# Optimization experiments

Hardware: AMD Instinct MI355X
Metric: run time of the kernel (lower is better)

## Reference

```python
import jax, jax.numpy as jnp
import numpy as np

N_NODES = 50000
N_EDGES = 1_600_000
DIMS = [3, 4096, 1024, 256, 64, 16]  # conv1..conv5 in/out widths


def setup_inputs() -> dict:
    key = jax.random.key(0)
    ks = jax.random.split(key, 2 + 2 * 6)
    x = jax.random.normal(ks[0], (N_NODES, DIMS[0]), jnp.float32)
    edge_index = jax.random.randint(ks[1], (2, N_EDGES), 0, N_NODES, jnp.int64)
    inp = {"x": x, "edge_index": edge_index}
    # GCNConv weights (lin has no bias fused; bias added after aggregation)
    for i in range(5):
        fi, fo = DIMS[i], DIMS[i + 1]
        inp[f"W{i+1}"] = jax.random.normal(ks[2 + 2 * i], (fi, fo), jnp.float32) / np.float32(np.sqrt(fi))
        inp[f"b{i+1}"] = jnp.zeros((fo,), jnp.float32)
    # final Linear(num_classes, 3)
    inp["Wl"] = jax.random.normal(ks[12], (DIMS[5], 3), jnp.float32) / np.float32(np.sqrt(DIMS[5]))
    inp["bl"] = jnp.zeros((3,), jnp.float32)
    return inp


def _gcn_layer(x, W, b, src, dst, dinv):
    """GCNConv: h = XW; out = D^-1/2 (A+I) D^-1/2 h + b (self-loops included)."""
    h = x @ W  # [N, out]
    norm = dinv[src] * dinv[dst]  # [E]
    agg = jax.ops.segment_sum(h[src] * norm[:, None], dst, num_segments=N_NODES)
    # self-loop term: norm_ii = dinv[i]^2
    return agg + h * (dinv * dinv)[:, None] + b


def reference(x, edge_index, W1, b1, W2, b2, W3, b3, W4, b4, W5, b5, Wl, bl):
    src, dst = edge_index[0], edge_index[1]
    # degree with self-loops (edge weights = 1), computed on target nodes
    deg = jax.ops.segment_sum(jnp.ones((N_EDGES,), x.dtype), dst, num_segments=N_NODES) + 1.0
    dinv = jax.lax.rsqrt(deg)
    h = _gcn_layer(x, W1, b1, src, dst, dinv)
    h = jax.nn.relu(h)  # dropout = identity in eval
    h = _gcn_layer(h, W2, b2, src, dst, dinv)
    h = jax.nn.relu(h)
    h = _gcn_layer(h, W3, b3, src, dst, dinv)
    h = jax.nn.relu(h)
    h = _gcn_layer(h, W4, b4, src, dst, dinv)
    h = jax.nn.relu(h)
    h = _gcn_layer(h, W5, b5, src, dst, dinv)
    # scatter_mean with broadcast index [0] -> global mean pool to [1, C]
    pooled = jnp.mean(h, axis=0, keepdims=True)
    return pooled @ Wl + bl  # [1, 3]
```

## Files before the change

### kernel.cpp

```cpp
#include <hip/hip_runtime.h>
#include <stdint.h>

#define NN 50000
#define NE 1600000

typedef _Float16 f16;
typedef __attribute__((ext_vector_type(8))) _Float16 h8;
typedef __attribute__((ext_vector_type(4))) _Float16 h4v;
typedef __attribute__((ext_vector_type(4))) float f32x4;
typedef __attribute__((ext_vector_type(2))) float f32x2;

union PackU { unsigned int u; f16 h[2]; };
union Pack4 { uint2 v; f16 h[4]; };
union Pack8 { uint4 v; f16 h[8]; };

__device__ __forceinline__ void storev(float* p, float v) { *p = v; }
__device__ __forceinline__ void storev(f16* p, float v) { *p = (f16)v; }

__device__ __forceinline__ unsigned char f2fp8(float v) {
    int pk = __builtin_amdgcn_cvt_pk_fp8_f32(v, v, 0, false);
    return (unsigned char)(pk & 0xff);
}

__global__ __launch_bounds__(256) void zero_int_kernel(int* __restrict__ p, int n) {
    int i = blockIdx.x * 256 + threadIdx.x;
    if (i < n) p[i] = 0;
}

__global__ __launch_bounds__(256) void count_kernel(const int* __restrict__ dst,
                                                    int* __restrict__ deg, int nE) {
    int e = blockIdx.x * 256 + threadIdx.x;
    if (e < nE) atomicAdd(&deg[dst[e]], 1);
}

__global__ __launch_bounds__(256) void dinv_kernel(const int* __restrict__ deg,
                                                   float* __restrict__ dinv, int n) {
    int i = blockIdx.x * 256 + threadIdx.x;
    if (i < n) dinv[i] = rsqrtf((float)deg[i] + 1.0f);
}

__global__ __launch_bounds__(256) void scan1_kernel(const int* __restrict__ cnt,
                                                    int* __restrict__ rs,
                                                    int* __restrict__ bsum, int n) {
    __shared__ int sm[256];
    int b = blockIdx.x, t = threadIdx.x, i = b * 256 + t;
    int v = (i < n) ? cnt[i] : 0;
    sm[t] = v;
    __syncthreads();
    for (int off = 1; off < 256; off <<= 1) {
        int x = 0;
        if (t >= off) x = sm[t - off];
        __syncthreads();
        if (t >= off) sm[t] += x;
        __syncthreads();
    }
    if (i < n) rs[i] = sm[t] - v;
    if (t == 255) bsum[b] = sm[255];
}

__global__ __launch_bounds__(256) void scan2_kernel(int* __restrict__ bsum,
                                                    int* __restrict__ rs, int nb, int n) {
    __shared__ int sm[256];
    int t = threadIdx.x;
    int v = (t < nb) ? bsum[t] : 0;
    sm[t] = v;
    __syncthreads();
    for (int off = 1; off < 256; off <<= 1) {
        int x = 0;
        if (t >= off) x = sm[t - off];
        __syncthreads();
        if (t >= off) sm[t] += x;
        __syncthreads();
    }
    if (t < nb) bsum[t] = sm[t] - v;
    if (t == 255) rs[n] = sm[255];
}

__global__ __launch_bounds__(256) void scan3_kernel(int* __restrict__ rs,
                                                    const int* __restrict__ bsum, int n) {
    int i = blockIdx.x * 256 + threadIdx.x;
    if (i < n) rs[i] += bsum[blockIdx.x];
}

__global__ __launch_bounds__(256) void fill_kernel(const int* __restrict__ src,
                                                   const int* __restrict__ dst,
                                                   const int* __restrict__ rs,
                                                   int* __restrict__ cur,
                                                   int* __restrict__ csr, int nE) {
    int e = blockIdx.x * 256 + threadIdx.x;
    if (e < nE) {
        int d = dst[e];
        int p = rs[d] + atomicAdd(&cur[d], 1);
        csr[p] = src[e];
    }
}

__global__ __launch_bounds__(256) void pack_w1_kernel(const float* __restrict__ W1,
                                                      const float* __restrict__ b1,
                                                      float* __restrict__ w1p) {
    int k = blockIdx.x * 256 + threadIdx.x;
    if (k < 4096) {
        w1p[k * 4 + 0] = W1[k];
        w1p[k * 4 + 1] = W1[4096 + k];
        w1p[k * 4 + 2] = W1[8192 + k];
        w1p[k * 4 + 3] = b1[k];
    }
}

__global__ __launch_bounds__(256) void tconv_kernel(const float* __restrict__ W,
                                                    f16* __restrict__ Wt,
                                                    int K, int N) {
    __shared__ float tile[32][33];
    int kb = blockIdx.y * 32, nb = blockIdx.x * 32;
    int tx = threadIdx.x & 31, ty = threadIdx.x >> 5;
    for (int r = ty; r < 32; r += 8)
        tile[r][tx] = W[(size_t)(kb + r) * N + nb + tx];
    __syncthreads();
    for (int r = ty; r < 32; r += 8)
        Wt[(size_t)(nb + r) * K + kb + tx] = (f16)tile[tx][r];
}

template <int F, int TPN, bool RELU, bool BIAS, typename OutT>
__global__ __launch_bounds__(256) void agg_kernel(const float* __restrict__ t,
                                                  const float* __restrict__ dinv,
                                                  const int* __restrict__ rs,
                                                  const int* __restrict__ csr,
                                                  const float* __restrict__ bias,
                                                  OutT* __restrict__ out, int out_ld,
                                                  int nNodes) {
    constexpr int NPB = 256 / TPN;
    constexpr int C   = F / TPN;
    static_assert(TPN * C == F, "F must be TPN*C");
    int node = blockIdx.x * NPB + (int)threadIdx.x / TPN;
    if (node >= nNodes) return;
    int lane = (int)threadIdx.x % TPN;

    float acc[C];
#pragma unroll
    for (int c = 0; c < C; ++c) acc[c] = 0.f;

    int e0 = rs[node], e1 = rs[node + 1];
    for (int e = e0; e < e1; ++e) {
        int s = csr[e];
        float w = dinv[s];
        const float* tr = t + (size_t)s * F;
#pragma unroll
        for (int c = 0; c < C; ++c) acc[c] += w * tr[lane + c * TPN];
    }
    float di = dinv[node];
    const float* ti = t + (size_t)node * F;
    OutT* oi = out + (size_t)node * out_ld;
#pragma unroll
    for (int c = 0; c < C; ++c) {
        int col = lane + c * TPN;
        float v = di * acc[c] + di * di * ti[col];
        if (BIAS) v += bias[col];
        if (RELU) v = fmaxf(v, 0.f);
        storev(oi + col, v);
    }
}

template <bool RELU>
__global__ __launch_bounds__(256) void agg_fp8_1024(const unsigned char* __restrict__ t,
                                                    const float* __restrict__ dinv,
                                                    const int* __restrict__ rs,
                                                    const int* __restrict__ csr,
                                                    const float* __restrict__ bias,
                                                    f16* __restrict__ out, int nNodes) {
    int node = blockIdx.x * 4 + ((int)threadIdx.x >> 6);
    if (node >= nNodes) return;
    int lane = (int)threadIdx.x & 63;

    float acc[16];
#pragma unroll
    for (int j = 0; j < 16; ++j) acc[j] = 0.f;

    int e0 = rs[node], e1 = rs[node + 1];
    int e = e0;
    for (; e + 1 < e1; e += 2) {
        int s0 = csr[e], s1 = csr[e + 1];
        float w0 = dinv[s0], w1 = dinv[s1];
        uint4 u0 = ((const uint4*)(t + (size_t)s0 * 1024))[lane];
        uint4 u1 = ((const uint4*)(t + (size_t)s1 * 1024))[lane];
        const unsigned int uw0[4] = {u0.x, u0.y, u0.z, u0.w};
        const unsigned int uw1[4] = {u1.x, u1.y, u1.z, u1.w};
#pragma unroll
        for (int q = 0; q < 4; ++q) {
            f32x2 l0 = __builtin_amdgcn_cvt_pk_f32_fp8((int)uw0[q], false);
            f32x2 h0 = __builtin_amdgcn_cvt_pk_f32_fp8((int)uw0[q], true);
            f32x2 l1 = __builtin_amdgcn_cvt_pk_f32_fp8((int)uw1[q], false);
            f32x2 h1 = __builtin_amdgcn_cvt_pk_f32_fp8((int)uw1[q], true);
            acc[q * 4 + 0] += w0 * l0.x + w1 * l1.x;
            acc[q * 4 + 1] += w0 * l0.y + w1 * l1.y;
            acc[q * 4 + 2] += w0 * h0.x + w1 * h1.x;
            acc[q * 4 + 3] += w0 * h0.y + w1 * h1.y;
        }
    }
    if (e < e1) {
        int s0 = csr[e];
        float w0 = dinv[s0];
        uint4 u0 = ((const uint4*)(t + (size_t)s0 * 1024))[lane];
        const unsigned int uw0[4] = {u0.x, u0.y, u0.z, u0.w};
#pragma unroll
        for (int q = 0; q < 4; ++q) {
            f32x2 l0 = __builtin_amdgcn_cvt_pk_f32_fp8((int)uw0[q], false);
            f32x2 h0 = __builtin_amdgcn_cvt_pk_f32_fp8((int)uw0[q], true);
            acc[q * 4 + 0] += w0 * l0.x;
            acc[q * 4 + 1] += w0 * l0.y;
            acc[q * 4 + 2] += w0 * h0.x;
            acc[q * 4 + 3] += w0 * h0.y;
        }
    }
    float di = dinv[node], di2 = di * di;
    uint4 us = ((const uint4*)(t + (size_t)node * 1024))[lane];
    const unsigned int uws[4] = {us.x, us.y, us.z, us.w};
    Pack8 o0, o1;
#pragma unroll
    for (int q = 0; q < 4; ++q) {
        f32x2 sl = __builtin_amdgcn_cvt_pk_f32_fp8((int)uws[q], false);
        f32x2 sh = __builtin_amdgcn_cvt_pk_f32_fp8((int)uws[q], true);
        float4 b = *(const float4*)(bias + 16 * lane + q * 4);
        float v0 = di * acc[q * 4 + 0] + di2 * sl.x + b.x;
        float v1 = di * acc[q * 4 + 1] + di2 * sl.y + b.y;
        float v2 = di * acc[q * 4 + 2] + di2 * sh.x + b.z;
        float v3 = di * acc[q * 4 + 3] + di2 * sh.y + b.w;
        if (RELU) {
            v0 = fmaxf(v0, 0.f); v1 = fmaxf(v1, 0.f);
            v2 = fmaxf(v2, 0.f); v3 = fmaxf(v3, 0.f);
        }
        Pack8& dst8 = (q < 2) ? o0 : o1;
        int base = (q & 1) * 4;
        dst8.h[base + 0] = (f16)v0;
        dst8.h[base + 1] = (f16)v1;
        dst8.h[base + 2] = (f16)v2;
        dst8.h[base + 3] = (f16)v3;
    }
    uint4* orow = (uint4*)(out + (size_t)node * 1024 + 16 * lane);
    orow[0] = o0.v;
    orow[1] = o1.v;
}

template <bool RELU>
__global__ __launch_bounds__(256) void agg_fp8_256(const unsigned char* __restrict__ t,
                                                   int in_ld,
                                                   const float* __restrict__ dinv,
                                                   const int* __restrict__ rs,
                                                   const int* __restrict__ csr,
                                                   const float* __restrict__ bias,
                                                   f16* __restrict__ out,
                                                   int out_ld, int nNodes) {
    int node = blockIdx.x * 4 + ((int)threadIdx.x >> 6);
    if (node >= nNodes) return;
    int lane = (int)threadIdx.x & 63;

    float acc0 = 0.f, acc1 = 0.f, acc2 = 0.f, acc3 = 0.f;
    int e0 = rs[node], e1 = rs[node + 1];
    int e = e0;
    for (; e + 1 < e1; e += 2) {
        int s0 = csr[e], s1 = csr[e + 1];
        float w0 = dinv[s0], w1 = dinv[s1];
        unsigned int u0 = ((const unsigned int*)(t + (size_t)s0 * in_ld))[lane];
        unsigned int u1 = ((const unsigned int*)(t + (size_t)s1 * in_ld))[lane];
        f32x2 l0 = __builtin_amdgcn_cvt_pk_f32_fp8((int)u0, false);
        f32x2 h0 = __builtin_amdgcn_cvt_pk_f32_fp8((int)u0, true);
        f32x2 l1 = __builtin_amdgcn_cvt_pk_f32_fp8((int)u1, false);
        f32x2 h1 = __builtin_amdgcn_cvt_pk_f32_fp8((int)u1, true);
        acc0 += w0 * l0.x + w1 * l1.x;
        acc1 += w0 * l0.y + w1 * l1.y;
        acc2 += w0 * h0.x + w1 * h1.x;
        acc3 += w0 * h0.y + w1 * h1.y;
    }
    if (e < e1) {
        int s0 = csr[e];
        float w0 = dinv[s0];
        unsigned int u0 = ((const unsigned int*)(t + (size_t)s0 * in_ld))[lane];
        f32x2 l0 = __builtin_amdgcn_cvt_pk_f32_fp8((int)u0, false);
        f32x2 h0 = __builtin_amdgcn_cvt_pk_f32_fp8((int)u0, true);
        acc0 += w0 * l0.x;
        acc1 += w0 * l0.y;
        acc2 += w0 * h0.x;
        acc3 += w0 * h0.y;
    }
    float di = dinv[node], di2 = di * di;
    unsigned int us = ((const unsigned int*)(t + (size_t)node * in_ld))[lane];
    f32x2 sl = __builtin_amdgcn_cvt_pk_f32_fp8((int)us, false);
    f32x2 sh = __builtin_amdgcn_cvt_pk_f32_fp8((int)us, true);
    float4 b = *(const float4*)(bias + 4 * lane);
    float v0 = di * acc0 + di2 * sl.x + b.x;
    float v1 = di * acc1 + di2 * sl.y + b.y;
    float v2 = di * acc2 + di2 * sh.x + b.z;
    float v3 = di * acc3 + di2 * sh.y + b.w;
    if (RELU) {
        v0 = fmaxf(v0, 0.f); v1 = fmaxf(v1, 0.f);
        v2 = fmaxf(v2, 0.f); v3 = fmaxf(v3, 0.f);
    }
    Pack4 pk;
    pk.h[0] = (f16)v0; pk.h[1] = (f16)v1; pk.h[2] = (f16)v2; pk.h[3] = (f16)v3;
    *(uint2*)(out + (size_t)node * out_ld + 4 * lane) = pk.v;
}

#define LDSTR 40

__global__ __launch_bounds__(512, 4) void gemm12_mfma4(const float* __restrict__ aggx,
                                                       const float* __restrict__ w1p,
                                                       const f16* __restrict__ Bt,
                                                       unsigned char* __restrict__ t2) {
    __shared__ f16 As[128 * LDSTR] __attribute__((aligned(16)));
    __shared__ f16 Bs[256 * LDSTR] __attribute__((aligned(16)));
    int tid = threadIdx.x;
    int m0  = blockIdx.x * 128;
    int n0c = blockIdx.y * 256;

    int mg = tid >> 3;
    int kg = tid & 7;
    float a0[2], a1[2], a2[2];
#pragma unroll
    for (int j = 0; j < 2; ++j) {
        int gm = m0 + mg * 2 + j;
        if (gm < NN) {
            a0[j] = aggx[gm * 3 + 0];
            a1[j] = aggx[gm * 3 + 1];
            a2[j] = aggx[gm * 3 + 2];
        } else {
            a0[j] = a1[j] = a2[j] = 0.f;
        }
    }

    int brow = tid >> 1;
    int bkof = (tid & 1) * 16;
    const f16* bbase = Bt + (size_t)(n0c + brow) * 4096 + bkof;

    int lane   = tid & 63;
    int wv     = tid >> 6;
    int wm     = (wv >> 2) * 64;
    int wn     = (wv & 3) * 64;
    int fr_m   = lane & 15;
    int khalf8 = (lane >> 4) * 8;

    h8 pb0 = *(const h8*)(bbase);
    h8 pb1 = *(const h8*)(bbase + 8);

    f32x4 acc[4][4];
#pragma unroll
    for (int i = 0; i < 4; ++i)
#pragma unroll
        for (int j = 0; j < 4; ++j) acc[i][j] = (f32x4){0.f, 0.f, 0.f, 0.f};

    for (int k0 = 0; k0 < 4096; k0 += 32) {
        int kb = k0 + kg * 4;
        float4 wk0 = *(const float4*)(w1p + (size_t)(kb + 0) * 4);
        float4 wk1 = *(const float4*)(w1p + (size_t)(kb + 1) * 4);
        float4 wk2 = *(const float4*)(w1p + (size_t)(kb + 2) * 4);
        float4 wk3 = *(const float4*)(w1p + (size_t)(kb + 3) * 4);
#pragma unroll
        for (int j = 0; j < 2; ++j) {
            float h0 = fmaxf(a0[j] * wk0.x + a1[j] * wk0.y + a2[j] * wk0.z + wk0.w, 0.f);
            float h1 = fmaxf(a0[j] * wk1.x + a1[j] * wk1.y + a2[j] * wk1.z + wk1.w, 0.f);
            float h2 = fmaxf(a0[j] * wk2.x + a1[j] * wk2.y + a2[j] * wk2.z + wk2.w, 0.f);
            float h3 = fmaxf(a0[j] * wk3.x + a1[j] * wk3.y + a2[j] * wk3.z + wk3.w, 0.f);
            Pack4 pk;
            pk.h[0] = (f16)h0; pk.h[1] = (f16)h1; pk.h[2] = (f16)h2; pk.h[3] = (f16)h3;
            *(uint2*)(&As[(mg * 2 + j) * LDSTR + kg * 4]) = pk.v;
        }
        *(h8*)(&Bs[brow * LDSTR + bkof]) = pb0;
        *(h8*)(&Bs[brow * LDSTR + bkof + 8]) = pb1;
        __syncthreads();

        int kn = k0 + 32;
        if (kn < 4096) {
            pb0 = *(const h8*)(bbase + kn);
            pb1 = *(const h8*)(bbase + kn + 8);
        }

        h8 af[4];
#pragma unroll
        for (int mt = 0; mt < 4; ++mt)
            af[mt] = *(const h8*)(&As[(wm + mt * 16 + fr_m) * LDSTR + khalf8]);
#pragma unroll
        for (int nt = 0; nt < 4; ++nt) {
            h8 bf = *(const h8*)(&Bs[(wn + nt * 16 + fr_m) * LDSTR + khalf8]);
#pragma unroll
            for (int mt = 0; mt < 4; ++mt)
                acc[mt][nt] = __builtin_amdgcn_mfma_f32_16x16x32_f16(af[mt], bf, acc[mt][nt], 0, 0, 0);
        }
        __syncthreads();
    }

#pragma unroll
    for (int mt = 0; mt < 4; ++mt) {
#pragma unroll
        for (int reg = 0; reg < 4; ++reg) {
            int gm = m0 + wm + mt * 16 + (lane >> 4) * 4 + reg;
            if (gm < NN) {
                unsigned char* orow = t2 + (size_t)gm * 1024 + n0c + wn + fr_m;
#pragma unroll
                for (int nt = 0; nt < 4; ++nt)
                    orow[nt * 16] = f2fp8(acc[mt][nt][reg]);
            }
        }
    }
}

__global__ __launch_bounds__(256) void gemm_mfma(const f16* __restrict__ A, int lda,
                                                 const f16* __restrict__ Bt, int K,
                                                 unsigned char* __restrict__ C, int ldc,
                                                 int M) {
    __shared__ f16 As[128 * LDSTR] __attribute__((aligned(16)));
    __shared__ f16 Bs[128 * LDSTR] __attribute__((aligned(16)));
    int tid = threadIdx.x;
    int m0 = blockIdx.y * 128;
    int n0 = blockIdx.x * 128;

    int row = tid >> 1;
    int kof = (tid & 1) * 16;
    int am  = m0 + row;
    if (am > M - 1) am = M - 1;

    int lane   = tid & 63;
    int wv     = tid >> 6;
    int fr_m   = lane & 15;
    int khalf8 = (lane >> 4) * 8;

    const f16* abase = A + (size_t)am * lda + kof;
    const f16* bbase = Bt + (size_t)(n0 + row) * K + kof;

    h8 pa0 = *(const h8*)(abase);
    h8 pa1 = *(const h8*)(abase + 8);
    h8 pb0 = *(const h8*)(bbase);
    h8 pb1 = *(const h8*)(bbase + 8);

    f32x4 acc[2][8];
#pragma unroll
    for (int i = 0; i < 2; ++i)
#pragma unroll
        for (int j = 0; j < 8; ++j) acc[i][j] = (f32x4){0.f, 0.f, 0.f, 0.f};

    for (int k0 = 0; k0 < K; k0 += 32) {
        *(h8*)(&As[row * LDSTR + kof]) = pa0;
        *(h8*)(&As[row * LDSTR + kof + 8]) = pa1;
        *(h8*)(&Bs[row * LDSTR + kof]) = pb0;
        *(h8*)(&Bs[row * LDSTR + kof + 8]) = pb1;
        __syncthreads();

        int kn = k0 + 32;
        if (kn < K) {
            pa0 = *(const h8*)(abase + kn);
            pa1 = *(const h8*)(abase + kn + 8);
            pb0 = *(const h8*)(bbase + kn);
            pb1 = *(const h8*)(bbase + kn + 8);
        }

        h8 af0 = *(const h8*)(&As[(wv * 32 + fr_m) * LDSTR + khalf8]);
        h8 af1 = *(const h8*)(&As[(wv * 32 + 16 + fr_m) * LDSTR + khalf8]);
#pragma unroll
        for (int nt = 0; nt < 8; ++nt) {
            h8 bf = *(const h8*)(&Bs[(nt * 16 + fr_m) * LDSTR + khalf8]);
            acc[0][nt] = __builtin_amdgcn_mfma_f32_16x16x32_f16(af0, bf, acc[0][nt], 0, 0, 0);
            acc[1][nt] = __builtin_amdgcn_mfma_f32_16x16x32_f16(af1, bf, acc[1][nt], 0, 0, 0);
        }
        __syncthreads();
    }

#pragma unroll
    for (int mt = 0; mt < 2; ++mt) {
#pragma unroll
        for (int reg = 0; reg < 4; ++reg) {
            int gm = m0 + wv * 32 + mt * 16 + (lane >> 4) * 4 + reg;
            if (gm < M) {
                unsigned char* orow = C + (size_t)gm * ldc + n0 + fr_m;
#pragma unroll
                for (int nt = 0; nt < 8; ++nt)
                    orow[nt * 16] = f2fp8(acc[mt][nt][reg]);
            }
        }
    }
}

#define BM 64
#define BN 64
#define BKS 16
__global__ __launch_bounds__(256) void gemm_f16A_kernel(const f16* __restrict__ A,
                                                        const float* __restrict__ B,
                                                        float* __restrict__ C,
                                                        int M, int K, int N) {
    __shared__ float As[BKS][BM + 4];
    __shared__ float Bs[BKS][BN + 4];
    int tid = threadIdx.x;
    int tx = tid & 15;
    int ty = tid >> 4;
    int m0 = blockIdx.y * BM;
    int n0 = blockIdx.x * BN;

    float acc[4][4];
#pragma unroll
    for (int i = 0; i < 4; ++i)
#pragma unroll
        for (int j = 0; j < 4; ++j) acc[i][j] = 0.f;

    int lmA = tid >> 2;
    int lkA = (tid & 3) * 4;
    int lkB = tid >> 4;
    int lnB = (tid & 15) * 4;

    for (int k0 = 0; k0 < K; k0 += BKS) {
        int gm = m0 + lmA;
        if (gm > M - 1) gm = M - 1;
        h4v av = *(const h4v*)(A + (size_t)gm * K + k0 + lkA);
        As[lkA + 0][lmA] = (float)av.x;
        As[lkA + 1][lmA] = (float)av.y;
        As[lkA + 2][lmA] = (float)av.z;
        As[lkA + 3][lmA] = (float)av.w;
        float4 bv = *reinterpret_cast<const float4*>(B + (size_t)(k0 + lkB) * N + n0 + lnB);
        *reinterpret_cast<float4*>(&Bs[lkB][lnB]) = bv;
        __syncthreads();

#pragma unroll
        for (int k = 0; k < BKS; ++k) {
            float4 a4 = *reinterpret_cast<const float4*>(&As[k][ty * 4]);
            float4 b4 = *reinterpret_cast<const float4*>(&Bs[k][tx * 4]);
            float a[4] = {a4.x, a4.y, a4.z, a4.w};
            float b[4] = {b4.x, b4.y, b4.z, b4.w};
#pragma unroll
            for (int i = 0; i < 4; ++i)
#pragma unroll
                for (int j = 0; j < 4; ++j) acc[i][j] += a[i] * b[j];
        }
        __syncthreads();
    }

#pragma unroll
    for (int i = 0; i < 4; ++i) {
        int m = m0 + ty * 4 + i;
        if (m < M) {
            float4 o = make_float4(acc[i][0], acc[i][1], acc[i][2], acc[i][3]);
            *reinterpret_cast<float4*>(C + (size_t)m * N + n0 + tx * 4) = o;
        }
    }
}

__global__ __launch_bounds__(256) void gemm5_kernel(const f16* __restrict__ h4,
                                                    const float* __restrict__ W5,
                                                    float* __restrict__ t5, int nNodes) {
    int idx = blockIdx.x * 256 + threadIdx.x;
    int i = idx >> 4, j = idx & 15;
    if (i >= nNodes) return;
    const f16* a = h4 + (size_t)i * 64;
    float s = 0.f;
#pragma unroll
    for (int k = 0; k < 64; ++k) s += (float)a[k] * W5[k * 16 + j];
    t5[idx] = s;
}

__global__ __launch_bounds__(256) void pool_kernel(const float* __restrict__ h5,
                                                   float* __restrict__ pool) {
    __shared__ float red[256];
    int c = blockIdx.x;
    float s = 0.f;
    for (int i = threadIdx.x; i < NN; i += 256) s += h5[(size_t)i * 16 + c];
    red[threadIdx.x] = s;
    __syncthreads();
    for (int off = 128; off > 0; off >>= 1) {
        if ((int)threadIdx.x < off) red[threadIdx.x] += red[threadIdx.x + off];
        __syncthreads();
    }
    if (threadIdx.x == 0) pool[c] = red[0];
}

__global__ void final_kernel(const float* __restrict__ pool, const float* __restrict__ Wl,
                             const float* __restrict__ bl, float* __restrict__ out) {
    int j = threadIdx.x;
    if (j < 3) {
        float s = 0.f;
#pragma unroll
        for (int c = 0; c < 16; ++c) s += pool[c] * Wl[c * 3 + j];
        out[j] = s * (1.0f / (float)NN) + bl[j];
    }
}

extern "C" void kernel_launch(void* const* d_in, const int* in_sizes, int n_in,
                              void* d_out, int out_size, void* d_ws, size_t ws_size,
                              hipStream_t stream) {
    (void)in_sizes; (void)n_in; (void)out_size; (void)ws_size;

    const float* x  = (const float*)d_in[0];
    const int*   ei = (const int*)d_in[1];
    const float* W1 = (const float*)d_in[2];
    const float* b1 = (const float*)d_in[3];
    const float* W2 = (const float*)d_in[4];
    const float* b2 = (const float*)d_in[5];
    const float* W3 = (const float*)d_in[6];
    const float* b3 = (const float*)d_in[7];
    const float* W4 = (const float*)d_in[8];
    const float* b4 = (const float*)d_in[9];
    const float* W5 = (const float*)d_in[10];
    const float* b5 = (const float*)d_in[11];
    const float* Wl = (const float*)d_in[12];
    const float* bl = (const float*)d_in[13];
    float* out = (float*)d_out;

    const int* srcp = ei;
    const int* dstp = ei + NE;

    char* p = (char*)d_ws;
    auto carve = [&](size_t bytes) {
        char* r = p;
        p += (bytes + 255) & ~(size_t)255;
        return r;
    };
    int*   deg  = (int*)carve(NN * 4);
    int*   cur  = (int*)carve(NN * 4);
    int*   rs   = (int*)carve((NN + 1) * 4);
    int*   bsum = (int*)carve(256 * 4);
    int*   csr  = (int*)carve((size_t)NE * 4);
    float* dinv = (float*)carve(NN * 4);
    float* aggx = (float*)carve((size_t)NN * 3 * 4);
    float* pool = (float*)carve(16 * 4);
    float* w1p  = (float*)carve((size_t)4096 * 4 * 4);
    f16*   w2t  = (f16*)carve((size_t)1024 * 4096 * 2);
    f16*   w3t  = (f16*)carve((size_t)256 * 1024 * 2);
    unsigned char* tbuf = (unsigned char*)carve((size_t)NN * 1024);
    f16*   h2   = (f16*)carve((size_t)NN * 1024 * 2);
    f16*   h3   = (f16*)carve((size_t)NN * 256 * 2);
    f16*   h4   = (f16*)carve((size_t)NN * 64 * 2);
    float* h5   = (float*)carve((size_t)NN * 16 * 4);
    float* tf32 = (float*)tbuf;

    const int NB = (NN + 255) / 256;

    zero_int_kernel<<<NB, 256, 0, stream>>>(deg, NN);
    zero_int_kernel<<<NB, 256, 0, stream>>>(cur, NN);
    count_kernel<<<(NE + 255) / 256, 256, 0, stream>>>(dstp, deg, NE);
    dinv_kernel<<<NB, 256, 0, stream>>>(deg, dinv, NN);
    scan1_kernel<<<NB, 256, 0, stream>>>(deg, rs, bsum, NN);
    scan2_kernel<<<1, 256, 0, stream>>>(bsum, rs, NB, NN);
    scan3_kernel<<<NB, 256, 0, stream>>>(rs, bsum, NN);
    fill_kernel<<<(NE + 255) / 256, 256, 0, stream>>>(srcp, dstp, rs, cur, csr, NE);

    pack_w1_kernel<<<16, 256, 0, stream>>>(W1, b1, w1p);
    tconv_kernel<<<dim3(1024 / 32, 4096 / 32), 256, 0, stream>>>(W2, w2t, 4096, 1024);
    tconv_kernel<<<dim3(256 / 32, 1024 / 32), 256, 0, stream>>>(W3, w3t, 1024, 256);

    agg_kernel<3, 1, false, false, float><<<NB, 256, 0, stream>>>(
        x, dinv, rs, csr, nullptr, aggx, 3, NN);

    const int MB2 = (NN + 127) / 128;

    gemm12_mfma4<<<dim3(MB2, 4), 512, 0, stream>>>(aggx, w1p, w2t, tbuf);
    agg_fp8_1024<true><<<(NN + 3) / 4, 256, 0, stream>>>(
        tbuf, dinv, rs, csr, b2, h2, NN);

    gemm_mfma<<<dim3(2, MB2), 256, 0, stream>>>(
        h2, 1024, w3t, 1024, tbuf, 256, NN);
    agg_fp8_256<true><<<(NN + 3) / 4, 256, 0, stream>>>(
        tbuf, 256, dinv, rs, csr, b3, h3, 256, NN);

    gemm_f16A_kernel<<<dim3(1, (NN + BM - 1) / BM), 256, 0, stream>>>(
        h3, W4, tf32, NN, 256, 64);
    agg_kernel<64, 64, true, true, f16><<<(NN + 3) / 4, 256, 0, stream>>>(
        tf32, dinv, rs, csr, b4, h4, 64, NN);

    gemm5_kernel<<<(NN * 16 + 255) / 256, 256, 0, stream>>>(h4, W5, tf32, NN);
    agg_kernel<16, 16, false, true, float><<<(NN + 15) / 16, 256, 0, stream>>>(
        tf32, dinv, rs, csr, b5, h5, 16, NN);

    pool_kernel<<<16, 256, 0, stream>>>(h5, pool);
    final_kernel<<<1, 64, 0, stream>>>(pool, Wl, bl, out);
}
```

Baseline: 1.636 ms.

## Double-buffer LDS in fused layer1-2 GEMM to drop one barrier per k-step

Converts the fused conv1+conv2 MFMA GEMM to ping-pong LDS buffers for A and B. The next k-tile is staged (B from registers, A recomputed from the layer-1 transform) while MFMAs run on the current buffer, and the global B prefetch is pushed two steps ahead. This cuts the barriers per iteration from two to one and overlaps LDS writes with compute. LDS use doubles to about 60 KB per block, which may reduce occupancy, and register pressure rises from the extra prefetch state.

Measured after the change: 1.597 ms. 1.02x faster.

```diff
diff --git a/kernel.cpp b/kernel.cpp
--- a/kernel.cpp
+++ b/kernel.cpp
@@ -301,12 +301,12 @@
 
 #define LDSTR 40
 
-__global__ __launch_bounds__(512, 4) void gemm12_mfma4(const float* __restrict__ aggx,
-                                                       const float* __restrict__ w1p,
-                                                       const f16* __restrict__ Bt,
-                                                       unsigned char* __restrict__ t2) {
-    __shared__ f16 As[128 * LDSTR] __attribute__((aligned(16)));
-    __shared__ f16 Bs[256 * LDSTR] __attribute__((aligned(16)));
+__global__ __launch_bounds__(512, 4) void gemm12_mfma10(const float* __restrict__ aggx,
+                                                        const float* __restrict__ w1p,
+                                                        const f16* __restrict__ Bt,
+                                                        unsigned char* __restrict__ t2) {
+    __shared__ f16 As[2 * 128 * LDSTR] __attribute__((aligned(16)));
+    __shared__ f16 Bs[2 * 256 * LDSTR] __attribute__((aligned(16)));
     int tid = threadIdx.x;
     int m0  = blockIdx.x * 128;
     int n0c = blockIdx.y * 256;
@@ -337,17 +337,8 @@
     int fr_m   = lane & 15;
     int khalf8 = (lane >> 4) * 8;
 
-    h8 pb0 = *(const h8*)(bbase);
-    h8 pb1 = *(const h8*)(bbase + 8);
-
-    f32x4 acc[4][4];
-#pragma unroll
-    for (int i = 0; i < 4; ++i)
-#pragma unroll
-        for (int j = 0; j < 4; ++j) acc[i][j] = (f32x4){0.f, 0.f, 0.f, 0.f};
-
-    for (int k0 = 0; k0 < 4096; k0 += 32) {
-        int kb = k0 + kg * 4;
+    auto stageA = [&](f16* dstAs, int kk) {
+        int kb = kk + kg * 4;
         float4 wk0 = *(const float4*)(w1p + (size_t)(kb + 0) * 4);
         float4 wk1 = *(const float4*)(w1p + (size_t)(kb + 1) * 4);
         float4 wk2 = *(const float4*)(w1p + (size_t)(kb + 2) * 4);
@@ -360,30 +351,58 @@
             float h3 = fmaxf(a0[j] * wk3.x + a1[j] * wk3.y + a2[j] * wk3.z + wk3.w, 0.f);
             Pack4 pk;
             pk.h[0] = (f16)h0; pk.h[1] = (f16)h1; pk.h[2] = (f16)h2; pk.h[3] = (f16)h3;
-            *(uint2*)(&As[(mg * 2 + j) * LDSTR + kg * 4]) = pk.v;
-        }
-        *(h8*)(&Bs[brow * LDSTR + bkof]) = pb0;
-        *(h8*)(&Bs[brow * LDSTR + bkof + 8]) = pb1;
-        __syncthreads();
-
-        int kn = k0 + 32;
-        if (kn < 4096) {
-            pb0 = *(const h8*)(bbase + kn);
-            pb1 = *(const h8*)(bbase + kn + 8);
+            *(uint2*)(&dstAs[(mg * 2 + j) * LDSTR + kg * 4]) = pk.v;
+        }
+    };
+
+    h8 pb0 = *(const h8*)(bbase);
+    h8 pb1 = *(const h8*)(bbase + 8);
+    stageA(As, 0);
+    *(h8*)(&Bs[brow * LDSTR + bkof]) = pb0;
+    *(h8*)(&Bs[brow * LDSTR + bkof + 8]) = pb1;
+    pb0 = *(const h8*)(bbase + 32);
+    pb1 = *(const h8*)(bbase + 32 + 8);
+
+    f32x4 acc[4][4];
+#pragma unroll
+    for (int i = 0; i < 4; ++i)
+#pragma unroll
+        for (int j = 0; j < 4; ++j) acc[i][j] = (f32x4){0.f, 0.f, 0.f, 0.f};
+
+    int p = 0;
+    for (int k0 = 0; k0 < 4096; k0 += 32) {
+        __syncthreads();
+        const f16* Asc = As + p * (128 * LDSTR);
+        const f16* Bsc = Bs + p * (256 * LDSTR);
+        f16* Asn = As + (p ^ 1) * (128 * LDSTR);
+        f16* Bsn = Bs + (p ^ 1) * (256 * LDSTR);
+
+        int k1 = k0 + 32;
+        if (k1 < 4096) {
+            *(h8*)(&Bsn[brow * LDSTR + bkof]) = pb0;
+            *(h8*)(&Bsn[brow * LDSTR + bkof + 8]) = pb1;
+            stageA(Asn, k1);
         }
 
         h8 af[4];
 #pragma unroll
         for (int mt = 0; mt < 4; ++mt)
-            af[mt] = *(const h8*)(&As[(wm + mt * 16 + fr_m) * LDSTR + khalf8]);
+            af[mt] = *(const h8*)(&Asc[(wm + mt * 16 + fr_m) * LDSTR + khalf8]);
+
+        int k2 = k0 + 64;
+        if (k2 < 4096) {
+            pb0 = *(const h8*)(bbase + k2);
+            pb1 = *(const h8*)(bbase + k2 + 8);
+        }
+
 #pragma unroll
         for (int nt = 0; nt < 4; ++nt) {
-            h8 bf = *(const h8*)(&Bs[(wn + nt * 16 + fr_m) * LDSTR + khalf8]);
+            h8 bf = *(const h8*)(&Bsc[(wn + nt * 16 + fr_m) * LDSTR + khalf8]);
 #pragma unroll
             for (int mt = 0; mt < 4; ++mt)
                 acc[mt][nt] = __builtin_amdgcn_mfma_f32_16x16x32_f16(af[mt], bf, acc[mt][nt], 0, 0, 0);
         }
-        __syncthreads();
+        p ^= 1;
     }
 
 #pragma unroll
@@ -645,7 +664,7 @@
 
     const int MB2 = (NN + 127) / 128;
 
-    gemm12_mfma4<<<dim3(MB2, 4), 512, 0, stream>>>(aggx, w1p, w2t, tbuf);
+    gemm12_mfma10<<<dim3(MB2, 4), 512, 0, stream>>>(aggx, w1p, w2t, tbuf);
     agg_fp8_1024<true><<<(NN + 3) / 4, 256, 0, stream>>>(
         tbuf, dinv, rs, csr, b2, h2, NN);
 
```
